# Performance work log

Measured on AMD Instinct MI355X. Metric: run time of the kernel, lower is better.

Reference implementation:

```python
import jax, jax.numpy as jnp
import numpy as np
import math

B, T, C, H = 2, 2048, 1024, 16
HD = C // H  # head_dim = 64


def setup_inputs() -> dict:
    key = jax.random.key(0)
    ks = jax.random.split(key, 10)
    s = 1.0 / math.sqrt(C)
    x = jax.random.normal(ks[0], (B, T, C), jnp.float32)
    wq = jax.random.normal(ks[1], (C, C), jnp.float32) * s
    wk = jax.random.normal(ks[2], (C, C), jnp.float32) * s
    wv = jax.random.normal(ks[3], (C, C), jnp.float32) * s
    wo = jax.random.normal(ks[4], (C, C), jnp.float32) * s
    bq = jnp.zeros((C,), jnp.float32)
    bk = jnp.zeros((C,), jnp.float32)
    bv = jnp.zeros((C,), jnp.float32)
    bo = jnp.zeros((C,), jnp.float32)
    fractal_dim = jnp.ones((1,), jnp.float32)  # scalar fractal dimension input
    alpha = jnp.asarray(1.5, jnp.float32)
    fractal_alpha_scale = jnp.asarray(0.5, jnp.float32)
    energy_normalizer = jnp.asarray(1.0, jnp.float32)
    return {"x": x, "fractal_dim": fractal_dim, "wq": wq, "bq": bq, "wk": wk,
            "bk": bk, "wv": wv, "bv": bv, "wo": wo, "bo": bo, "alpha": alpha,
            "fractal_alpha_scale": fractal_alpha_scale,
            "energy_normalizer": energy_normalizer}


def reference(x, fractal_dim, wq, bq, wk, bk, wv, bv, wo, bo, alpha,
              fractal_alpha_scale, energy_normalizer):
    b, t, c = x.shape
    # input energy: L2 norm over channels, [b, t, 1]
    input_energy = jnp.linalg.norm(x, axis=-1, keepdims=True)
    adaptive_alpha = alpha + fractal_alpha_scale * (fractal_dim - 1.5)  # [1]

    q = (x @ wq + bq).reshape(b, t, H, HD)
    k = (x @ wk + bk).reshape(b, t, H, HD)
    v = (x @ wv + bv).reshape(b, t, H, HD)

    # per-head FFT along the time axis -> complex64
    q_fft = jnp.fft.fft(q, axis=1)
    k_fft = jnp.fft.fft(k, axis=1)
    v_fft = jnp.fft.fft(v, axis=1)

    freqs = jnp.fft.fftfreq(t).astype(jnp.float32)  # [t]
    phase = adaptive_alpha * jnp.arctan(jnp.log(jnp.abs(freqs) + 1e-10))  # [t]
    # unit-modulus complex spectral filter, broadcast [1, t, 1, 1]
    filt = jax.lax.complex(jnp.cos(phase), jnp.sin(phase))[None, :, None, None]

    qf = q_fft * filt
    kf = k_fft * filt
    vf = v_fft * filt

    # real part of complex matmul Q_f @ K_f^T, computed without complex GEMM:
    # Re(qf kf^T) = qr kr^T - qi ki^T
    inv_sqrt = np.float32(1.0 / math.sqrt(HD))
    logits = (jnp.einsum('bthd,bshd->bhts', qf.real, kf.real)
              - jnp.einsum('bthd,bshd->bhts', qf.imag, kf.imag)) * inv_sqrt
    attn = jax.nn.softmax(logits, axis=-1)  # [b, h, t, s]

    # attn is real, so Re(attn @ vf) = attn @ Re(vf); out_proj has real weights
    # so taking the real part before the projection is exact.
    attended = jnp.einsum('bhts,bshd->bthd', attn, vf.real)
    out = attended.reshape(b, t, c) @ wo + bo

    out_energy = jnp.linalg.norm(out, axis=-1, keepdims=True)
    energy_ratio = input_energy / (out_energy + 1e-8)
    return out * energy_ratio * energy_normalizer
```

## Files before the change

### kernel.cpp

```cpp
#include <hip/hip_runtime.h>
#include <math.h>


typedef _Float16 half8 __attribute__((ext_vector_type(8)));
typedef float f32x4 __attribute__((ext_vector_type(4)));
#define MFMA16 __builtin_amdgcn_mfma_f32_16x16x32_f16

#define GLOAD16(g, l) __builtin_amdgcn_global_load_lds( \
    (const __attribute__((address_space(1))) void*)(g), \
    (__attribute__((address_space(3))) void*)(l), 16, 0, 0)

__device__ inline unsigned pack_split(float v) {
    _Float16 h = (_Float16)v;
    float r = (v - (float)h) * 2048.0f;
    _Float16 l = (_Float16)r;
    union { _Float16 f; unsigned short u; } a, b;
    a.f = h; b.f = l;
    return (unsigned)a.u | ((unsigned)b.u << 16);
}
__device__ inline void split2(float v, _Float16& h, _Float16& l) {
    h = (_Float16)v;
    l = (_Float16)((v - (float)h) * 2048.0f);
}
__device__ inline _Float16 lo16(unsigned u) {
    union { unsigned short s; _Float16 f; } x; x.s = (unsigned short)(u & 0xffffu); return x.f;
}
__device__ inline _Float16 hi16(unsigned u) {
    union { unsigned short s; _Float16 f; } x; x.s = (unsigned short)(u >> 16); return x.f;
}

__device__ inline void write_split(_Float16* dh, _Float16* dl, uint4 u0, uint4 u1) {
    uint4 lo, hi;
    lo.x = __builtin_amdgcn_perm(u0.y, u0.x, 0x05040100u);
    lo.y = __builtin_amdgcn_perm(u0.w, u0.z, 0x05040100u);
    lo.z = __builtin_amdgcn_perm(u1.y, u1.x, 0x05040100u);
    lo.w = __builtin_amdgcn_perm(u1.w, u1.z, 0x05040100u);
    hi.x = __builtin_amdgcn_perm(u0.y, u0.x, 0x07060302u);
    hi.y = __builtin_amdgcn_perm(u0.w, u0.z, 0x07060302u);
    hi.z = __builtin_amdgcn_perm(u1.y, u1.x, 0x07060302u);
    hi.w = __builtin_amdgcn_perm(u1.w, u1.z, 0x07060302u);
    *(uint4*)dh = lo;
    *(uint4*)dl = hi;
}

__global__ __launch_bounds__(256) void k_init_tables(
    float2* __restrict__ tw, float2* __restrict__ filt,
    const float* __restrict__ fd, const float* __restrict__ alpha,
    const float* __restrict__ fas)
{
    int i = blockIdx.x * 256 + threadIdx.x;
    double aa = (double)alpha[0] + (double)fas[0] * ((double)fd[0] - 1.5);
    if (i < 1024) {
        double ang = -2.0 * 3.14159265358979323846 * (double)i / 2048.0;
        double s, c;
        sincos(ang, &s, &c);
        tw[i] = make_float2((float)c, (float)s);
    }
    if (i < 2048) {
        double fr = (i < 1024) ? (double)i / 2048.0 : ((double)i - 2048.0) / 2048.0;
        double ph = aa * atan(log(fabs(fr) + 1e-10));
        double s, c;
        sincos(ph, &s, &c);
        filt[i] = make_float2((float)c, (float)s);
    }
}

__global__ __launch_bounds__(256) void k_prep_wpl3(
    const float* __restrict__ wq, const float* __restrict__ wk,
    const float* __restrict__ wv, _Float16* __restrict__ wpl)
{
    __shared__ float tile[64][65];
    const int z = blockIdx.z;
    const float* W = (z == 0) ? wq : (z == 1) ? wk : wv;
    _Float16* Whi = wpl + (size_t)z * 2097152;
    _Float16* Wlo = Whi + 1048576;
    const int kb = blockIdx.x * 64, cb = blockIdx.y * 64;
    const int t = threadIdx.x, r = t >> 4, c4 = (t & 15) * 4;
#pragma unroll
    for (int i = 0; i < 4; ++i) {
        int row = r + 16 * i;
        float4 v = *(const float4*)&W[(size_t)(kb + row) * 1024 + cb + c4];
        tile[row][c4 + 0] = v.x; tile[row][c4 + 1] = v.y;
        tile[row][c4 + 2] = v.z; tile[row][c4 + 3] = v.w;
    }
    __syncthreads();
#pragma unroll
    for (int h = 0; h < 2; ++h) {
        int idx = t + h * 256;
        int lane = idx & 63, kt2 = (idx >> 6) & 1, ct = idx >> 7;
        int cl = ct * 16 + (lane & 15);
        int kl = kt2 * 32 + ((lane >> 4) * 8);
        half8 hv, lv;
#pragma unroll
        for (int j = 0; j < 8; ++j) {
            _Float16 hh, ll;
            split2(tile[kl + j][cl], hh, ll);
            hv[j] = hh; lv[j] = ll;
        }
        size_t u = ((size_t)((cb >> 4) + ct) * 32 + (kb >> 5) + kt2) * 64 + lane;
        *(half8*)&Whi[u * 8] = hv;
        *(half8*)&Wlo[u * 8] = lv;
    }
}

__global__ __launch_bounds__(256) void k_prep_xpl(
    const float* __restrict__ x, _Float16* __restrict__ xpl)
{
    __shared__ float tile[64][65];
    _Float16* Xhi = xpl;
    _Float16* Xlo = xpl + 4194304;
    const int nb = blockIdx.x * 64, cb = blockIdx.y * 64;
    const int t = threadIdx.x, r = t >> 4, c4 = (t & 15) * 4;
#pragma unroll
    for (int i = 0; i < 4; ++i) {
        int row = r + 16 * i;
        float4 v = *(const float4*)&x[(size_t)(nb + row) * 1024 + cb + c4];
        tile[row][c4 + 0] = v.x; tile[row][c4 + 1] = v.y;
        tile[row][c4 + 2] = v.z; tile[row][c4 + 3] = v.w;
    }
    __syncthreads();
#pragma unroll
    for (int h = 0; h < 2; ++h) {
        int idx = t + h * 256;
        int lane = idx & 63, ct2 = (idx >> 6) & 1, ntl = (idx >> 7) & 3;
        int nl = ntl * 16 + (lane & 15);
        int cl = ct2 * 32 + ((lane >> 4) * 8);
        half8 hv, lv;
#pragma unroll
        for (int j = 0; j < 8; ++j) {
            _Float16 hh, ll;
            split2(tile[nl][cl + j], hh, ll);
            hv[j] = hh; lv[j] = ll;
        }
        size_t u = ((size_t)((nb >> 4) + ntl) * 32 + (cb >> 5) + ct2) * 64 + lane;
        *(half8*)&Xhi[u * 8] = hv;
        *(half8*)&Xlo[u * 8] = lv;
    }
}

__global__ __launch_bounds__(256) void k_prep_w(
    const float* __restrict__ W, unsigned* __restrict__ Wpk)
{
    __shared__ float tile[64][65];
    const int kb = blockIdx.x * 64, cb = blockIdx.y * 64;
    const int t = threadIdx.x, r = t >> 4, c4 = (t & 15) * 4;
#pragma unroll
    for (int i = 0; i < 4; ++i) {
        int row = r + 16 * i;
        float4 v = *(const float4*)&W[(size_t)(kb + row) * 1024 + cb + c4];
        tile[row][c4 + 0] = v.x; tile[row][c4 + 1] = v.y;
        tile[row][c4 + 2] = v.z; tile[row][c4 + 3] = v.w;
    }
    __syncthreads();
#pragma unroll
    for (int i = 0; i < 4; ++i) {
        int crow = r + 16 * i;
        uint4 o;
        o.x = pack_split(tile[c4 + 0][crow]);
        o.y = pack_split(tile[c4 + 1][crow]);
        o.z = pack_split(tile[c4 + 2][crow]);
        o.w = pack_split(tile[c4 + 3][crow]);
        *(uint4*)&Wpk[(size_t)(cb + crow) * 1024 + kb + c4] = o;
    }
}

__global__ __launch_bounds__(256) void k_gemm_qkv(
    const _Float16* __restrict__ xpl, const _Float16* __restrict__ wpl,
    const float* __restrict__ bq, const float* __restrict__ bk,
    const float* __restrict__ bv,
    float* __restrict__ qT, float* __restrict__ kT, float* __restrict__ vT)
{
    __shared__ __align__(16) _Float16 Ab[2][8][2][64][8];
    __shared__ __align__(16) _Float16 Bb[2][8][2][64][8];
    const int tid = threadIdx.x;
    const int mat = blockIdx.z;
    const _Float16* Ahi = wpl + (size_t)mat * 2097152;
    const _Float16* Alo = Ahi + 1048576;
    const _Float16* Bhi = xpl;
    const _Float16* Blo = xpl + 4194304;
    const float* bias = (mat == 0) ? bq : (mat == 1) ? bk : bv;
    float* outp       = (mat == 0) ? qT : (mat == 1) ? kT : vT;
    const int m0 = blockIdx.x * 128, n0 = blockIdx.y * 128;
    const int w = tid >> 6, lane = tid & 63, quad = lane >> 4, l15 = lane & 15;
    const int wm = (w & 1) * 4, wn = (w >> 1) * 4;

    const int s0 = 2 * w, s1 = 2 * w + 1;
    const size_t aT0 = (size_t)((m0 >> 4) + s0) * 32;
    const size_t aT1 = aT0 + 32;
    const size_t bT0 = (size_t)((n0 >> 4) + s0) * 32;
    const size_t bT1 = bT0 + 32;
    const int ln8 = lane * 8;

    f32x4 acc1[4][4], acc2[4][4];
    const f32x4 z4 = {0.f, 0.f, 0.f, 0.f};
#pragma unroll
    for (int i = 0; i < 4; ++i)
#pragma unroll
        for (int j = 0; j < 4; ++j) { acc1[i][j] = z4; acc2[i][j] = z4; }

    {
        size_t oA0 = aT0 * 512 + ln8;
        size_t oA1 = aT1 * 512 + ln8;
        size_t oB0 = bT0 * 512 + ln8;
        size_t oB1 = bT1 * 512 + ln8;
        GLOAD16(Ahi + oA0, &Ab[0][s0][0][0][0]);
        GLOAD16(Alo + oA0, &Ab[0][s0][1][0][0]);
        GLOAD16(Ahi + oA1, &Ab[0][s1][0][0][0]);
        GLOAD16(Alo + oA1, &Ab[0][s1][1][0][0]);
        GLOAD16(Bhi + oB0, &Bb[0][s0][0][0][0]);
        GLOAD16(Blo + oB0, &Bb[0][s0][1][0][0]);
        GLOAD16(Bhi + oB1, &Bb[0][s1][0][0][0]);
        GLOAD16(Blo + oB1, &Bb[0][s1][1][0][0]);
    }
    __syncthreads();

    for (int kt = 0; kt < 32; ++kt) {
        const int cur = kt & 1, nxt = cur ^ 1;
        if (kt < 31) {
            int kn = kt + 1;
            size_t oA0 = (aT0 + kn) * 512 + ln8;
            size_t oA1 = (aT1 + kn) * 512 + ln8;
            size_t oB0 = (bT0 + kn) * 512 + ln8;
            size_t oB1 = (bT1 + kn) * 512 + ln8;
            GLOAD16(Ahi + oA0, &Ab[nxt][s0][0][0][0]);
            GLOAD16(Alo + oA0, &Ab[nxt][s0][1][0][0]);
            GLOAD16(Ahi + oA1, &Ab[nxt][s1][0][0][0]);
            GLOAD16(Alo + oA1, &Ab[nxt][s1][1][0][0]);
            GLOAD16(Bhi + oB0, &Bb[nxt][s0][0][0][0]);
            GLOAD16(Blo + oB0, &Bb[nxt][s0][1][0][0]);
            GLOAD16(Bhi + oB1, &Bb[nxt][s1][0][0][0]);
            GLOAD16(Blo + oB1, &Bb[nxt][s1][1][0][0]);
        }
        half8 ah[4], al[4];
#pragma unroll
        for (int mt = 0; mt < 4; ++mt) {
            ah[mt] = *(half8*)&Ab[cur][wm + mt][0][lane][0];
            al[mt] = *(half8*)&Ab[cur][wm + mt][1][lane][0];
        }
#pragma unroll
        for (int nt = 0; nt < 4; ++nt) {
            half8 bh = *(half8*)&Bb[cur][wn + nt][0][lane][0];
            half8 bl = *(half8*)&Bb[cur][wn + nt][1][lane][0];
#pragma unroll
            for (int mt = 0; mt < 4; ++mt) {
                acc1[mt][nt] = MFMA16(ah[mt], bh, acc1[mt][nt], 0, 0, 0);
                acc2[mt][nt] = MFMA16(ah[mt], bl, acc2[mt][nt], 0, 0, 0);
                acc2[mt][nt] = MFMA16(al[mt], bh, acc2[mt][nt], 0, 0, 0);
            }
        }
        __syncthreads();
    }
    const int b_ = n0 >> 11, t0 = n0 & 2047;
#pragma unroll
    for (int mt = 0; mt < 4; ++mt) {
#pragma unroll
        for (int r_ = 0; r_ < 4; ++r_) {
            int m = m0 + (wm + mt) * 16 + quad * 4 + r_;
            float bs = bias[m];
            float* orow = &outp[(size_t)(b_ * 1024 + m) * 2048 + t0];
#pragma unroll
            for (int nt = 0; nt < 4; ++nt) {
                float val = acc1[mt][nt][r_] + acc2[mt][nt][r_] * (1.f / 2048.f) + bs;
                orow[(wn + nt) * 16 + l15] = val;
            }
        }
    }
}

__global__ __launch_bounds__(256) void k_fft_filter(
    float* __restrict__ qT, float* __restrict__ kT, float* __restrict__ vT,
    float* __restrict__ qiT, float* __restrict__ kiT,
    const float2* __restrict__ tw, const float2* __restrict__ filt)
{
    __shared__ float2 sf[2048];
    const int bid = blockIdx.x;
    const int mat = bid >> 10;
    const int pair = bid & 1023;
    const int seq0 = pair * 2, seq1 = seq0 + 1;
    float* base = (mat == 0) ? qT : (mat == 1) ? kT : vT;
    float* src0 = base + (size_t)seq0 * 2048;
    float* src1 = base + (size_t)seq1 * 2048;
    const int tid = threadIdx.x;

    for (int i = tid; i < 2048; i += 256) {
        int j = (int)(__brev((unsigned)i) >> 21);
        sf[j] = make_float2(src0[i], src1[i]);
    }
    __syncthreads();
    for (int st = 1; st <= 11; ++st) {
        const int half = 1 << (st - 1);
        const int shift = 11 - st;
        for (int u = tid; u < 1024; u += 256) {
            int pos = u & (half - 1);
            int bi = 2 * u - pos;
            float2 w = tw[pos << shift];
            float2 a = sf[bi], b = sf[bi + half];
            float tr = w.x * b.x - w.y * b.y;
            float ti = w.x * b.y + w.y * b.x;
            sf[bi]        = make_float2(a.x + tr, a.y + ti);
            sf[bi + half] = make_float2(a.x - tr, a.y - ti);
        }
        __syncthreads();
    }
    unsigned* dr0 = (unsigned*)src0;
    unsigned* dr1 = (unsigned*)src1;
    unsigned* di0 = (mat == 0) ? (unsigned*)(qiT + (size_t)seq0 * 2048)
                               : (unsigned*)(kiT + (size_t)seq0 * 2048);
    unsigned* di1 = (mat == 0) ? (unsigned*)(qiT + (size_t)seq1 * 2048)
                               : (unsigned*)(kiT + (size_t)seq1 * 2048);
    for (int i = tid; i < 2048; i += 256) {
        float2 z  = sf[i];
        float2 zm = sf[(2048 - i) & 2047];
        float Are = 0.5f * (z.x + zm.x), Aim = 0.5f * (z.y - zm.y);
        float Bre = 0.5f * (z.y + zm.y), Bim = 0.5f * (zm.x - z.x);
        float2 f = filt[i];
        float re0 = Are * f.x - Aim * f.y, im0 = Are * f.y + Aim * f.x;
        float re1 = Bre * f.x - Bim * f.y, im1 = Bre * f.y + Bim * f.x;
        if (mat == 0) {
            dr0[i] = pack_split(0.125f * re0); di0[i] = pack_split(0.125f * im0);
            dr1[i] = pack_split(0.125f * re1); di1[i] = pack_split(0.125f * im1);
        } else if (mat == 1) {
            dr0[i] = pack_split(re0); di0[i] = pack_split(-im0);
            dr1[i] = pack_split(re1); di1[i] = pack_split(-im1);
        } else {
            dr0[i] = pack_split(re0);
            dr1[i] = pack_split(re1);
        }
    }
}

__global__ __launch_bounds__(512, 2) void k_flash(
    const unsigned* __restrict__ qpk, const unsigned* __restrict__ qipk,
    const unsigned* __restrict__ kpk, const unsigned* __restrict__ kipk,
    const unsigned* __restrict__ vpk, unsigned* __restrict__ attpk)
{
    __shared__ __align__(16) _Float16 Kbuf[2][4][4][2][64][8];
    __shared__ __align__(16) _Float16 Vbuf[2][2][4][2][64][8];

    const int tid = threadIdx.x;
    const int w = tid >> 6, lane = tid & 63;
    const int quad = lane >> 4, l15 = lane & 15;
    const int p = blockIdx.x;
    const int bh = (p & 7) * 4 + (p >> 6);
    const int tb = (p >> 3) & 7;
    const size_t bc = (size_t)bh * 64;
    const int tw0 = tb * 256 + w * 16;

    half8 aqh[2][4], aql[2][4];
#pragma unroll
    for (int rg = 0; rg < 2; ++rg) {
#pragma unroll
        for (int kc = 0; kc < 4; ++kc) {
#pragma unroll
            for (int j = 0; j < 8; ++j) {
                int d = kc * 32 + quad * 8 + j;
                int t = tw0 + rg * 128 + l15;
                unsigned u = (d < 64) ? qpk[(bc + d) * 2048 + t]
                                      : qipk[(bc + d - 64) * 2048 + t];
                aqh[rg][kc][j] = lo16(u);
                aql[rg][kc][j] = hi16(u);
            }
        }
    }

    f32x4 O1[2][4], O2[2][4];
    const f32x4 zero4 = {0.f, 0.f, 0.f, 0.f};
#pragma unroll
    for (int rg = 0; rg < 2; ++rg)
#pragma unroll
        for (int nt = 0; nt < 4; ++nt) { O1[rg][nt] = zero4; O2[rg][nt] = zero4; }
    float m_[2] = {-3e38f, -3e38f};
    float l_[2] = {0.f, 0.f};

    const int sK = tid & 63;
    const int dc0 = tid >> 6;
    const int stK = sK >> 4;
    const int kcK0 = dc0 >> 2;
    const int laneK = (sK & 15) + ((dc0 & 3) << 4);
    const unsigned* kre = &kpk[(bc + dc0 * 8) * 2048 + sK];
    const unsigned* kim = &kipk[(bc + dc0 * 8) * 2048 + sK];
    const int sc2V = tid >> 8;
    const int ntV = (tid >> 6) & 3, laneV = tid & 63;
    const int dV = ntV * 16 + (laneV & 15);
    const int s0V = sc2V * 32 + (laneV >> 4) * 4;
    const unsigned* vbase = &vpk[(bc + dV) * 2048 + s0V];

    unsigned ka0, ka1, ka2, ka3, ka4, ka5, ka6, ka7;
    unsigned kb0, kb1, kb2, kb3, kb4, kb5, kb6, kb7;
    uint4 va0, va1;
    ka0 = kre[0 * 2048]; ka1 = kre[1 * 2048];
    ka2 = kre[2 * 2048]; ka3 = kre[3 * 2048];
    ka4 = kre[4 * 2048]; ka5 = kre[5 * 2048];
    ka6 = kre[6 * 2048]; ka7 = kre[7 * 2048];
    kb0 = kim[0 * 2048]; kb1 = kim[1 * 2048];
    kb2 = kim[2 * 2048]; kb3 = kim[3 * 2048];
    kb4 = kim[4 * 2048]; kb5 = kim[5 * 2048];
    kb6 = kim[6 * 2048]; kb7 = kim[7 * 2048];
    va0 = *(const uint4*)vbase;
    va1 = *(const uint4*)(vbase + 16);
    write_split(&Kbuf[0][stK][kcK0][0][laneK][0], &Kbuf[0][stK][kcK0][1][laneK][0],
                make_uint4(ka0, ka1, ka2, ka3), make_uint4(ka4, ka5, ka6, ka7));
    write_split(&Kbuf[0][stK][kcK0 + 2][0][laneK][0], &Kbuf[0][stK][kcK0 + 2][1][laneK][0],
                make_uint4(kb0, kb1, kb2, kb3), make_uint4(kb4, kb5, kb6, kb7));
    write_split(&Vbuf[0][sc2V][ntV][0][laneV][0], &Vbuf[0][sc2V][ntV][1][laneV][0],
                va0, va1);
    kre += 64; kim += 64; vbase += 64;
    ka0 = kre[0 * 2048]; ka1 = kre[1 * 2048];
    ka2 = kre[2 * 2048]; ka3 = kre[3 * 2048];
    ka4 = kre[4 * 2048]; ka5 = kre[5 * 2048];
    ka6 = kre[6 * 2048]; ka7 = kre[7 * 2048];
    kb0 = kim[0 * 2048]; kb1 = kim[1 * 2048];
    kb2 = kim[2 * 2048]; kb3 = kim[3 * 2048];
    kb4 = kim[4 * 2048]; kb5 = kim[5 * 2048];
    kb6 = kim[6 * 2048]; kb7 = kim[7 * 2048];
    va0 = *(const uint4*)vbase;
    va1 = *(const uint4*)(vbase + 16);
    __syncthreads();

    for (int it = 0; it < 32; ++it) {
        const int cur = it & 1, nxt = cur ^ 1;
        if (it < 31) {
            write_split(&Kbuf[nxt][stK][kcK0][0][laneK][0],
                        &Kbuf[nxt][stK][kcK0][1][laneK][0],
                        make_uint4(ka0, ka1, ka2, ka3), make_uint4(ka4, ka5, ka6, ka7));
            write_split(&Kbuf[nxt][stK][kcK0 + 2][0][laneK][0],
                        &Kbuf[nxt][stK][kcK0 + 2][1][laneK][0],
                        make_uint4(kb0, kb1, kb2, kb3), make_uint4(kb4, kb5, kb6, kb7));
            write_split(&Vbuf[nxt][sc2V][ntV][0][laneV][0],
                        &Vbuf[nxt][sc2V][ntV][1][laneV][0], va0, va1);
        }
        if (it < 30) {
            kre += 64; kim += 64; vbase += 64;
            ka0 = kre[0 * 2048]; ka1 = kre[1 * 2048];
            ka2 = kre[2 * 2048]; ka3 = kre[3 * 2048];
            ka4 = kre[4 * 2048]; ka5 = kre[5 * 2048];
            ka6 = kre[6 * 2048]; ka7 = kre[7 * 2048];
            kb0 = kim[0 * 2048]; kb1 = kim[1 * 2048];
            kb2 = kim[2 * 2048]; kb3 = kim[3 * 2048];
            kb4 = kim[4 * 2048]; kb5 = kim[5 * 2048];
            kb6 = kim[6 * 2048]; kb7 = kim[7 * 2048];
            va0 = *(const uint4*)vbase;
            va1 = *(const uint4*)(vbase + 16);
        }

        f32x4 S1[2][4], S2[2][4];
#pragma unroll
        for (int rg = 0; rg < 2; ++rg)
#pragma unroll
            for (int st = 0; st < 4; ++st) { S1[rg][st] = zero4; S2[rg][st] = zero4; }
        __builtin_amdgcn_s_setprio(1);
#pragma unroll
        for (int st = 0; st < 4; ++st) {
#pragma unroll
            for (int kc = 0; kc < 4; ++kc) {
                half8 khf = *(half8*)&Kbuf[cur][st][kc][0][lane][0];
                half8 klf = *(half8*)&Kbuf[cur][st][kc][1][lane][0];
#pragma unroll
                for (int rg = 0; rg < 2; ++rg) {
                    S1[rg][st] = MFMA16(khf, aqh[rg][kc], S1[rg][st], 0, 0, 0);
                    S2[rg][st] = MFMA16(klf, aqh[rg][kc], S2[rg][st], 0, 0, 0);
                    S2[rg][st] = MFMA16(khf, aql[rg][kc], S2[rg][st], 0, 0, 0);
                }
            }
        }
        __builtin_amdgcn_s_setprio(0);

        half8 pb[2][2];
#pragma unroll
        for (int rg = 0; rg < 2; ++rg) {
#pragma unroll
            for (int st = 0; st < 4; ++st)
                S1[rg][st] = S1[rg][st] + S2[rg][st] * (1.f / 2048.f);
            float mt = -3e38f;
#pragma unroll
            for (int st = 0; st < 4; ++st)
#pragma unroll
                for (int r = 0; r < 4; ++r)
                    mt = fmaxf(mt, S1[rg][st][r]);
            mt = fmaxf(mt, __shfl_xor(mt, 16));
            mt = fmaxf(mt, __shfl_xor(mt, 32));
            if (!__all(mt <= m_[rg] + 8.f)) {
                float mn2 = fmaxf(m_[rg], mt);
                float al = __expf(m_[rg] - mn2);
                m_[rg] = mn2;
                l_[rg] *= al;
#pragma unroll
                for (int nt = 0; nt < 4; ++nt) { O1[rg][nt] *= al; O2[rg][nt] *= al; }
            }
            float mn = m_[rg];
            float rs = 0.f;
            _Float16 ph[4][4];
#pragma unroll
            for (int st = 0; st < 4; ++st)
#pragma unroll
                for (int r = 0; r < 4; ++r) {
                    float pe = __expf(S1[rg][st][r] - mn);
                    rs += pe;
                    ph[st][r] = (_Float16)pe;
                }
            rs += __shfl_xor(rs, 16);
            rs += __shfl_xor(rs, 32);
            l_[rg] += rs;
#pragma unroll
            for (int sc2 = 0; sc2 < 2; ++sc2) {
                half8 t8;
                t8[0] = ph[2 * sc2][0];     t8[1] = ph[2 * sc2][1];
                t8[2] = ph[2 * sc2][2];     t8[3] = ph[2 * sc2][3];
                t8[4] = ph[2 * sc2 + 1][0]; t8[5] = ph[2 * sc2 + 1][1];
                t8[6] = ph[2 * sc2 + 1][2]; t8[7] = ph[2 * sc2 + 1][3];
                pb[rg][sc2] = t8;
            }
        }

        __builtin_amdgcn_s_setprio(1);
#pragma unroll
        for (int sc2 = 0; sc2 < 2; ++sc2) {
#pragma unroll
            for (int nt = 0; nt < 4; ++nt) {
                half8 vh = *(half8*)&Vbuf[cur][sc2][nt][0][lane][0];
                half8 vl = *(half8*)&Vbuf[cur][sc2][nt][1][lane][0];
                O1[0][nt] = MFMA16(vh, pb[0][sc2], O1[0][nt], 0, 0, 0);
                O2[0][nt] = MFMA16(vl, pb[0][sc2], O2[0][nt], 0, 0, 0);
                O1[1][nt] = MFMA16(vh, pb[1][sc2], O1[1][nt], 0, 0, 0);
                O2[1][nt] = MFMA16(vl, pb[1][sc2], O2[1][nt], 0, 0, 0);
            }
        }
        __builtin_amdgcn_s_setprio(0);

        __syncthreads();
    }

    const int b = bh >> 4, h = bh & 15;
#pragma unroll
    for (int rg = 0; rg < 2; ++rg) {
        float inv = 1.0f / l_[rg];
        int t = tw0 + rg * 128 + l15;
        size_t row = (size_t)b * 2048 + t;
#pragma unroll
        for (int nt = 0; nt < 4; ++nt) {
#pragma unroll
            for (int r = 0; r < 4; ++r) {
                float val = (O1[rg][nt][r] + O2[rg][nt][r] * (1.f / 2048.f)) * inv;
                attpk[row * 1024 + h * 64 + nt * 16 + quad * 4 + r] = pack_split(val);
            }
        }
    }
}

__global__ __launch_bounds__(256) void k_gemm_out(
    const unsigned* __restrict__ attpk, const unsigned* __restrict__ wopk,
    const float* __restrict__ bo, float* __restrict__ out)
{
    __shared__ __align__(16) _Float16 Ab[8][2][64][8];
    __shared__ __align__(16) _Float16 Bb[8][2][64][8];
    const int tid = threadIdx.x;
    const int m0 = blockIdx.x * 128, n0 = blockIdx.y * 128;
    const int w = tid >> 6, lane = tid & 63, quad = lane >> 4, l15 = lane & 15;
    const int wm = (w & 1) * 4, wn = (w >> 1) * 4;

    const int chA = tid & 3, rA = tid >> 2;
    const int flA = (rA & 15) + 16 * chA, mtA = rA >> 4;
    const unsigned* gA0 = &attpk[(size_t)(m0 + rA) * 1024 + chA * 8];
    const unsigned* gA1 = gA0 + (size_t)64 * 1024;
    const unsigned* gB0 = &wopk[(size_t)(n0 + rA) * 1024 + chA * 8];
    const unsigned* gB1 = gB0 + (size_t)64 * 1024;

    uint4 pa0 = *(const uint4*)gA0, pa1 = *(const uint4*)(gA0 + 4);
    uint4 pa2 = *(const uint4*)gA1, pa3 = *(const uint4*)(gA1 + 4);
    uint4 pb0 = *(const uint4*)gB0, pb1 = *(const uint4*)(gB0 + 4);
    uint4 pb2 = *(const uint4*)gB1, pb3 = *(const uint4*)(gB1 + 4);

    f32x4 acc1[4][4], acc2[4][4];
    const f32x4 z4 = {0.f, 0.f, 0.f, 0.f};
#pragma unroll
    for (int i = 0; i < 4; ++i)
#pragma unroll
        for (int j = 0; j < 4; ++j) { acc1[i][j] = z4; acc2[i][j] = z4; }

    for (int k0 = 0; k0 < 1024; k0 += 32) {
        __syncthreads();
        write_split(&Ab[mtA][0][flA][0],     &Ab[mtA][1][flA][0],     pa0, pa1);
        write_split(&Ab[mtA + 4][0][flA][0], &Ab[mtA + 4][1][flA][0], pa2, pa3);
        write_split(&Bb[mtA][0][flA][0],     &Bb[mtA][1][flA][0],     pb0, pb1);
        write_split(&Bb[mtA + 4][0][flA][0], &Bb[mtA + 4][1][flA][0], pb2, pb3);
        __syncthreads();
        if (k0 < 992) {
            int kn = k0 + 32;
            pa0 = *(const uint4*)(gA0 + kn); pa1 = *(const uint4*)(gA0 + kn + 4);
            pa2 = *(const uint4*)(gA1 + kn); pa3 = *(const uint4*)(gA1 + kn + 4);
            pb0 = *(const uint4*)(gB0 + kn); pb1 = *(const uint4*)(gB0 + kn + 4);
            pb2 = *(const uint4*)(gB1 + kn); pb3 = *(const uint4*)(gB1 + kn + 4);
        }
        half8 ah[4], al[4];
#pragma unroll
        for (int mt = 0; mt < 4; ++mt) {
            ah[mt] = *(half8*)&Ab[wm + mt][0][lane][0];
            al[mt] = *(half8*)&Ab[wm + mt][1][lane][0];
        }
#pragma unroll
        for (int nt = 0; nt < 4; ++nt) {
            half8 bh = *(half8*)&Bb[wn + nt][0][lane][0];
            half8 bl = *(half8*)&Bb[wn + nt][1][lane][0];
#pragma unroll
            for (int mt = 0; mt < 4; ++mt) {
                acc1[mt][nt] = MFMA16(ah[mt], bh, acc1[mt][nt], 0, 0, 0);
                acc2[mt][nt] = MFMA16(ah[mt], bl, acc2[mt][nt], 0, 0, 0);
                acc2[mt][nt] = MFMA16(al[mt], bh, acc2[mt][nt], 0, 0, 0);
            }
        }
    }
#pragma unroll
    for (int mt = 0; mt < 4; ++mt) {
#pragma unroll
        for (int r_ = 0; r_ < 4; ++r_) {
            int m = m0 + (wm + mt) * 16 + quad * 4 + r_;
            float* orow = &out[(size_t)m * 1024 + n0];
#pragma unroll
            for (int nt = 0; nt < 4; ++nt) {
                int n = (wn + nt) * 16 + l15;
                float val = acc1[mt][nt][r_] + acc2[mt][nt][r_] * (1.f / 2048.f)
                          + bo[n0 + n];
                orow[n] = val;
            }
        }
    }
}

__global__ __launch_bounds__(256) void k_norm(
    const float* __restrict__ x, float* __restrict__ out,
    const float* __restrict__ en)
{
    const int row = blockIdx.x;
    const int tid = threadIdx.x;
    const float* xr = x + (size_t)row * 1024;
    float* orow = out + (size_t)row * 1024;
    float4 xv = *(const float4*)&xr[tid * 4];
    float4 ov = *(const float4*)&orow[tid * 4];
    float ssx = xv.x * xv.x + xv.y * xv.y + xv.z * xv.z + xv.w * xv.w;
    float sso = ov.x * ov.x + ov.y * ov.y + ov.z * ov.z + ov.w * ov.w;
#pragma unroll
    for (int m = 1; m <= 32; m <<= 1) {
        ssx += __shfl_xor(ssx, m, 64);
        sso += __shfl_xor(sso, m, 64);
    }
    __shared__ float rx[4], ro[4];
    const int wid = tid >> 6;
    if ((tid & 63) == 0) { rx[wid] = ssx; ro[wid] = sso; }
    __syncthreads();
    float tsx = rx[0] + rx[1] + rx[2] + rx[3];
    float tso = ro[0] + ro[1] + ro[2] + ro[3];
    float scale = sqrtf(tsx) / (sqrtf(tso) + 1e-8f) * en[0];
    ov.x *= scale; ov.y *= scale; ov.z *= scale; ov.w *= scale;
    *(float4*)&orow[tid * 4] = ov;
}

extern "C" void kernel_launch(void* const* d_in, const int* in_sizes, int n_in,
                              void* d_out, int out_size, void* d_ws, size_t ws_size,
                              hipStream_t stream)
{
    const float* x     = (const float*)d_in[0];
    const float* fd    = (const float*)d_in[1];
    const float* wq    = (const float*)d_in[2];
    const float* bq    = (const float*)d_in[3];
    const float* wk    = (const float*)d_in[4];
    const float* bk    = (const float*)d_in[5];
    const float* wv    = (const float*)d_in[6];
    const float* bv    = (const float*)d_in[7];
    const float* wo    = (const float*)d_in[8];
    const float* bo    = (const float*)d_in[9];
    const float* alpha = (const float*)d_in[10];
    const float* fas   = (const float*)d_in[11];
    const float* en    = (const float*)d_in[12];
    float* out = (float*)d_out;
    float* ws  = (float*)d_ws;

    float* qT  = ws;
    float* kT  = ws + (size_t)1 * 4194304;
    float* vT  = ws + (size_t)2 * 4194304;
    float* qiT = ws + (size_t)3 * 4194304;
    float* kiT = ws + (size_t)4 * 4194304;
    float* att = ws + (size_t)5 * 4194304;
    float2* tw   = (float2*)(ws + (size_t)6 * 4194304);
    float2* filt = (float2*)(ws + (size_t)6 * 4194304 + 2048);

    _Float16* wpl = (_Float16*)qiT;
    _Float16* xpl = (_Float16*)att;
    unsigned* attpk  = (unsigned*)att;
    unsigned* wopk   = (unsigned*)qT;

    k_init_tables<<<8, 256, 0, stream>>>(tw, filt, fd, alpha, fas);
    k_prep_wpl3<<<dim3(16, 16, 3), 256, 0, stream>>>(wq, wk, wv, wpl);
    k_prep_xpl<<<dim3(64, 16), 256, 0, stream>>>(x, xpl);
    k_gemm_qkv<<<dim3(8, 32, 3), 256, 0, stream>>>(xpl, wpl, bq, bk, bv,
                                                   qT, kT, vT);
    k_fft_filter<<<3072, 256, 0, stream>>>(qT, kT, vT, qiT, kiT, tw, filt);
    k_flash<<<256, 512, 0, stream>>>((const unsigned*)qT, (const unsigned*)qiT,
                                     (const unsigned*)kT, (const unsigned*)kiT,
                                     (const unsigned*)vT, attpk);
    k_prep_w<<<dim3(16, 16), 256, 0, stream>>>(wo, wopk);
    k_gemm_out<<<dim3(32, 8), 256, 0, stream>>>(attpk, wopk, bo, out);
    k_norm<<<4096, 256, 0, stream>>>(x, out, en);
}
```

Measured before the change: 424.5 us.

## Use MFMA-tiled planar fp16 layout for out-proj GEMM and radix-4 FFT stages

```diff
diff --git a/kernel.cpp b/kernel.cpp
--- a/kernel.cpp
+++ b/kernel.cpp
@@ -3,6 +3,7 @@
 
 
 typedef _Float16 half8 __attribute__((ext_vector_type(8)));
+typedef _Float16 half4 __attribute__((ext_vector_type(4)));
 typedef float f32x4 __attribute__((ext_vector_type(4)));
 #define MFMA16 __builtin_amdgcn_mfma_f32_16x16x32_f16
 
@@ -10,23 +11,25 @@
     (const __attribute__((address_space(1))) void*)(g), \
     (__attribute__((address_space(3))) void*)(l), 16, 0, 0)
 
+__device__ inline void split2(float v, _Float16& h, _Float16& l) {
+    h = (_Float16)v;
+    l = (_Float16)((v - (float)h) * 2048.0f);
+}
 __device__ inline unsigned pack_split(float v) {
-    _Float16 h = (_Float16)v;
-    float r = (v - (float)h) * 2048.0f;
-    _Float16 l = (_Float16)r;
+    _Float16 h, l;
+    split2(v, h, l);
     union { _Float16 f; unsigned short u; } a, b;
     a.f = h; b.f = l;
     return (unsigned)a.u | ((unsigned)b.u << 16);
 }
-__device__ inline void split2(float v, _Float16& h, _Float16& l) {
-    h = (_Float16)v;
-    l = (_Float16)((v - (float)h) * 2048.0f);
-}
 __device__ inline _Float16 lo16(unsigned u) {
     union { unsigned short s; _Float16 f; } x; x.s = (unsigned short)(u & 0xffffu); return x.f;
 }
 __device__ inline _Float16 hi16(unsigned u) {
     union { unsigned short s; _Float16 f; } x; x.s = (unsigned short)(u >> 16); return x.f;
+}
+__device__ inline float2 cmul(float2 a, float2 b) {
+    return make_float2(a.x * b.x - a.y * b.y, a.x * b.y + a.y * b.x);
 }
 
 __device__ inline void write_split(_Float16* dh, _Float16* dl, uint4 u0, uint4 u1) {
@@ -103,6 +106,41 @@
     }
 }
 
+__global__ __launch_bounds__(256) void k_prep_wpl1(
+    const float* __restrict__ W, _Float16* __restrict__ wpl)
+{
+    __shared__ float tile[64][65];
+    _Float16* Whi = wpl;
+    _Float16* Wlo = wpl + 1048576;
+    const int kb = blockIdx.x * 64, cb = blockIdx.y * 64;
+    const int t = threadIdx.x, r = t >> 4, c4 = (t & 15) * 4;
+#pragma unroll
+    for (int i = 0; i < 4; ++i) {
+        int row = r + 16 * i;
+        float4 v = *(const float4*)&W[(size_t)(kb + row) * 1024 + cb + c4];
+        tile[row][c4 + 0] = v.x; tile[row][c4 + 1] = v.y;
+        tile[row][c4 + 2] = v.z; tile[row][c4 + 3] = v.w;
+    }
+    __syncthreads();
+#pragma unroll
+    for (int h = 0; h < 2; ++h) {
+        int idx = t + h * 256;
+        int lane = idx & 63, kt2 = (idx >> 6) & 1, ct = idx >> 7;
+        int cl = ct * 16 + (lane & 15);
+        int kl = kt2 * 32 + ((lane >> 4) * 8);
+        half8 hv, lv;
+#pragma unroll
+        for (int j = 0; j < 8; ++j) {
+            _Float16 hh, ll;
+            split2(tile[kl + j][cl], hh, ll);
+            hv[j] = hh; lv[j] = ll;
+        }
+        size_t u = ((size_t)((cb >> 4) + ct) * 32 + (kb >> 5) + kt2) * 64 + lane;
+        *(half8*)&Whi[u * 8] = hv;
+        *(half8*)&Wlo[u * 8] = lv;
+    }
+}
+
 __global__ __launch_bounds__(256) void k_prep_xpl(
     const float* __restrict__ x, _Float16* __restrict__ xpl)
 {
@@ -135,32 +173,6 @@
         size_t u = ((size_t)((nb >> 4) + ntl) * 32 + (cb >> 5) + ct2) * 64 + lane;
         *(half8*)&Xhi[u * 8] = hv;
         *(half8*)&Xlo[u * 8] = lv;
-    }
-}
-
-__global__ __launch_bounds__(256) void k_prep_w(
-    const float* __restrict__ W, unsigned* __restrict__ Wpk)
-{
-    __shared__ float tile[64][65];
-    const int kb = blockIdx.x * 64, cb = blockIdx.y * 64;
-    const int t = threadIdx.x, r = t >> 4, c4 = (t & 15) * 4;
-#pragma unroll
-    for (int i = 0; i < 4; ++i) {
-        int row = r + 16 * i;
-        float4 v = *(const float4*)&W[(size_t)(kb + row) * 1024 + cb + c4];
-        tile[row][c4 + 0] = v.x; tile[row][c4 + 1] = v.y;
-        tile[row][c4 + 2] = v.z; tile[row][c4 + 3] = v.w;
-    }
-    __syncthreads();
-#pragma unroll
-    for (int i = 0; i < 4; ++i) {
-        int crow = r + 16 * i;
-        uint4 o;
-        o.x = pack_split(tile[c4 + 0][crow]);
-        o.y = pack_split(tile[c4 + 1][crow]);
-        o.z = pack_split(tile[c4 + 2][crow]);
-        o.w = pack_split(tile[c4 + 3][crow]);
-        *(uint4*)&Wpk[(size_t)(cb + crow) * 1024 + kb + c4] = o;
     }
 }
 
@@ -287,21 +299,41 @@
         sf[j] = make_float2(src0[i], src1[i]);
     }
     __syncthreads();
-    for (int st = 1; st <= 11; ++st) {
-        const int half = 1 << (st - 1);
-        const int shift = 11 - st;
-        for (int u = tid; u < 1024; u += 256) {
-            int pos = u & (half - 1);
-            int bi = 2 * u - pos;
-            float2 w = tw[pos << shift];
-            float2 a = sf[bi], b = sf[bi + half];
-            float tr = w.x * b.x - w.y * b.y;
-            float ti = w.x * b.y + w.y * b.x;
-            sf[bi]        = make_float2(a.x + tr, a.y + ti);
-            sf[bi + half] = make_float2(a.x - tr, a.y - ti);
+#pragma unroll
+    for (int st = 1; st <= 9; st += 2) {
+        const int h = 1 << (st - 1);
+        const int s = 11 - st;
+        for (int u = tid; u < 512; u += 256) {
+            int m = u & (h - 1);
+            int g = u >> (st - 1);
+            int bi = g * 4 * h + m;
+            float2 a = sf[bi], b = sf[bi + h], c = sf[bi + 2 * h], d = sf[bi + 3 * h];
+            float2 W  = tw[m << s];
+            float2 W2 = tw[m << (s - 1)];
+            float2 wb = cmul(W, b), wd = cmul(W, d);
+            float2 a1 = make_float2(a.x + wb.x, a.y + wb.y);
+            float2 b1 = make_float2(a.x - wb.x, a.y - wb.y);
+            float2 c1 = make_float2(c.x + wd.x, c.y + wd.y);
+            float2 d1 = make_float2(c.x - wd.x, c.y - wd.y);
+            float2 w2c = cmul(W2, c1);
+            float2 w2d = cmul(W2, d1);
+            float2 w3d = make_float2(w2d.y, -w2d.x);
+            sf[bi]         = make_float2(a1.x + w2c.x, a1.y + w2c.y);
+            sf[bi + 2 * h] = make_float2(a1.x - w2c.x, a1.y - w2c.y);
+            sf[bi + h]     = make_float2(b1.x + w3d.x, b1.y + w3d.y);
+            sf[bi + 3 * h] = make_float2(b1.x - w3d.x, b1.y - w3d.y);
         }
         __syncthreads();
     }
+    for (int u = tid; u < 1024; u += 256) {
+        float2 w = tw[u];
+        float2 a = sf[u], b = sf[u + 1024];
+        float2 wb = cmul(w, b);
+        sf[u]        = make_float2(a.x + wb.x, a.y + wb.y);
+        sf[u + 1024] = make_float2(a.x - wb.x, a.y - wb.y);
+    }
+    __syncthreads();
+
     unsigned* dr0 = (unsigned*)src0;
     unsigned* dr1 = (unsigned*)src1;
     unsigned* di0 = (mat == 0) ? (unsigned*)(qiT + (size_t)seq0 * 2048)
@@ -332,7 +364,7 @@
 __global__ __launch_bounds__(512, 2) void k_flash(
     const unsigned* __restrict__ qpk, const unsigned* __restrict__ qipk,
     const unsigned* __restrict__ kpk, const unsigned* __restrict__ kipk,
-    const unsigned* __restrict__ vpk, unsigned* __restrict__ attpk)
+    const unsigned* __restrict__ vpk, _Float16* __restrict__ attpl)
 {
     __shared__ __align__(16) _Float16 Kbuf[2][4][4][2][64][8];
     __shared__ __align__(16) _Float16 Vbuf[2][2][4][2][64][8];
@@ -534,41 +566,48 @@
 #pragma unroll
     for (int rg = 0; rg < 2; ++rg) {
         float inv = 1.0f / l_[rg];
-        int t = tw0 + rg * 128 + l15;
-        size_t row = (size_t)b * 2048 + t;
+        int mrow = b * 2048 + tw0 + rg * 128 + l15;
+        size_t mt32 = (size_t)(mrow >> 4) * 32;
 #pragma unroll
         for (int nt = 0; nt < 4; ++nt) {
+            size_t u = (mt32 + h * 2 + (nt >> 1)) * 512
+                     + (size_t)(l15 + 16 * ((nt * 2 + (quad >> 1)) & 3)) * 8
+                     + (quad & 1) * 4;
+            half4 hv, lv;
 #pragma unroll
             for (int r = 0; r < 4; ++r) {
                 float val = (O1[rg][nt][r] + O2[rg][nt][r] * (1.f / 2048.f)) * inv;
-                attpk[row * 1024 + h * 64 + nt * 16 + quad * 4 + r] = pack_split(val);
-            }
+                _Float16 hh, ll;
+                split2(val, hh, ll);
+                hv[r] = hh; lv[r] = ll;
+            }
+            *(half4*)&attpl[u] = hv;
+            *(half4*)&attpl[4194304 + u] = lv;
         }
     }
 }
 
 __global__ __launch_bounds__(256) void k_gemm_out(
-    const unsigned* __restrict__ attpk, const unsigned* __restrict__ wopk,
+    const _Float16* __restrict__ attpl, const _Float16* __restrict__ wopl,
     const float* __restrict__ bo, float* __restrict__ out)
 {
-    __shared__ __align__(16) _Float16 Ab[8][2][64][8];
-    __shared__ __align__(16) _Float16 Bb[8][2][64][8];
+    __shared__ __align__(16) _Float16 Ab[2][8][2][64][8];
+    __shared__ __align__(16) _Float16 Bb[2][8][2][64][8];
     const int tid = threadIdx.x;
+    const _Float16* Ahi = attpl;
+    const _Float16* Alo = attpl + 4194304;
+    const _Float16* Bhi = wopl;
+    const _Float16* Blo = wopl + 1048576;
     const int m0 = blockIdx.x * 128, n0 = blockIdx.y * 128;
     const int w = tid >> 6, lane = tid & 63, quad = lane >> 4, l15 = lane & 15;
     const int wm = (w & 1) * 4, wn = (w >> 1) * 4;
 
-    const int chA = tid & 3, rA = tid >> 2;
-    const int flA = (rA & 15) + 16 * chA, mtA = rA >> 4;
-    const unsigned* gA0 = &attpk[(size_t)(m0 + rA) * 1024 + chA * 8];
-    const unsigned* gA1 = gA0 + (size_t)64 * 1024;
-    const unsigned* gB0 = &wopk[(size_t)(n0 + rA) * 1024 + chA * 8];
-    const unsigned* gB1 = gB0 + (size_t)64 * 1024;
-
-    uint4 pa0 = *(const uint4*)gA0, pa1 = *(const uint4*)(gA0 + 4);
-    uint4 pa2 = *(const uint4*)gA1, pa3 = *(const uint4*)(gA1 + 4);
-    uint4 pb0 = *(const uint4*)gB0, pb1 = *(const uint4*)(gB0 + 4);
-    uint4 pb2 = *(const uint4*)gB1, pb3 = *(const uint4*)(gB1 + 4);
+    const int s0 = 2 * w, s1 = 2 * w + 1;
+    const size_t aT0 = (size_t)((m0 >> 4) + s0) * 32;
+    const size_t aT1 = aT0 + 32;
+    const size_t bT0 = (size_t)((n0 >> 4) + s0) * 32;
+    const size_t bT1 = bT0 + 32;
+    const int ln8 = lane * 8;
 
     f32x4 acc1[4][4], acc2[4][4];
     const f32x4 z4 = {0.f, 0.f, 0.f, 0.f};
@@ -577,30 +616,49 @@
 #pragma unroll
         for (int j = 0; j < 4; ++j) { acc1[i][j] = z4; acc2[i][j] = z4; }
 
-    for (int k0 = 0; k0 < 1024; k0 += 32) {
-        __syncthreads();
-        write_split(&Ab[mtA][0][flA][0],     &Ab[mtA][1][flA][0],     pa0, pa1);
-        write_split(&Ab[mtA + 4][0][flA][0], &Ab[mtA + 4][1][flA][0], pa2, pa3);
-        write_split(&Bb[mtA][0][flA][0],     &Bb[mtA][1][flA][0],     pb0, pb1);
-        write_split(&Bb[mtA + 4][0][flA][0], &Bb[mtA + 4][1][flA][0], pb2, pb3);
-        __syncthreads();
-        if (k0 < 992) {
-            int kn = k0 + 32;
-            pa0 = *(const uint4*)(gA0 + kn); pa1 = *(const uint4*)(gA0 + kn + 4);
-            pa2 = *(const uint4*)(gA1 + kn); pa3 = *(const uint4*)(gA1 + kn + 4);
-            pb0 = *(const uint4*)(gB0 + kn); pb1 = *(const uint4*)(gB0 + kn + 4);
-            pb2 = *(const uint4*)(gB1 + kn); pb3 = *(const uint4*)(gB1 + kn + 4);
+    {
+        size_t oA0 = aT0 * 512 + ln8;
+        size_t oA1 = aT1 * 512 + ln8;
+        size_t oB0 = bT0 * 512 + ln8;
+        size_t oB1 = bT1 * 512 + ln8;
+        GLOAD16(Ahi + oA0, &Ab[0][s0][0][0][0]);
+        GLOAD16(Alo + oA0, &Ab[0][s0][1][0][0]);
+        GLOAD16(Ahi + oA1, &Ab[0][s1][0][0][0]);
+        GLOAD16(Alo + oA1, &Ab[0][s1][1][0][0]);
+        GLOAD16(Bhi + oB0, &Bb[0][s0][0][0][0]);
+        GLOAD16(Blo + oB0, &Bb[0][s0][1][0][0]);
+        GLOAD16(Bhi + oB1, &Bb[0][s1][0][0][0]);
+        GLOAD16(Blo + oB1, &Bb[0][s1][1][0][0]);
+    }
+    __syncthreads();
+
+    for (int kt = 0; kt < 32; ++kt) {
+        const int cur = kt & 1, nxt = cur ^ 1;
+        if (kt < 31) {
+            int kn = kt + 1;
+            size_t oA0 = (aT0 + kn) * 512 + ln8;
+            size_t oA1 = (aT1 + kn) * 512 + ln8;
+            size_t oB0 = (bT0 + kn) * 512 + ln8;
+            size_t oB1 = (bT1 + kn) * 512 + ln8;
+            GLOAD16(Ahi + oA0, &Ab[nxt][s0][0][0][0]);
+            GLOAD16(Alo + oA0, &Ab[nxt][s0][1][0][0]);
+            GLOAD16(Ahi + oA1, &Ab[nxt][s1][0][0][0]);
+            GLOAD16(Alo + oA1, &Ab[nxt][s1][1][0][0]);
+            GLOAD16(Bhi + oB0, &Bb[nxt][s0][0][0][0]);
+            GLOAD16(Blo + oB0, &Bb[nxt][s0][1][0][0]);
+            GLOAD16(Bhi + oB1, &Bb[nxt][s1][0][0][0]);
+            GLOAD16(Blo + oB1, &Bb[nxt][s1][1][0][0]);
         }
         half8 ah[4], al[4];
 #pragma unroll
         for (int mt = 0; mt < 4; ++mt) {
-            ah[mt] = *(half8*)&Ab[wm + mt][0][lane][0];
-            al[mt] = *(half8*)&Ab[wm + mt][1][lane][0];
+            ah[mt] = *(half8*)&Ab[cur][wm + mt][0][lane][0];
+            al[mt] = *(half8*)&Ab[cur][wm + mt][1][lane][0];
         }
 #pragma unroll
         for (int nt = 0; nt < 4; ++nt) {
-            half8 bh = *(half8*)&Bb[wn + nt][0][lane][0];
-            half8 bl = *(half8*)&Bb[wn + nt][1][lane][0];
+            half8 bh = *(half8*)&Bb[cur][wn + nt][0][lane][0];
+            half8 bl = *(half8*)&Bb[cur][wn + nt][1][lane][0];
 #pragma unroll
             for (int mt = 0; mt < 4; ++mt) {
                 acc1[mt][nt] = MFMA16(ah[mt], bh, acc1[mt][nt], 0, 0, 0);
@@ -608,6 +666,7 @@
                 acc2[mt][nt] = MFMA16(al[mt], bh, acc2[mt][nt], 0, 0, 0);
             }
         }
+        __syncthreads();
     }
 #pragma unroll
     for (int mt = 0; mt < 4; ++mt) {
@@ -683,10 +742,10 @@
     float2* tw   = (float2*)(ws + (size_t)6 * 4194304);
     float2* filt = (float2*)(ws + (size_t)6 * 4194304 + 2048);
 
-    _Float16* wpl = (_Float16*)qiT;
-    _Float16* xpl = (_Float16*)att;
-    unsigned* attpk  = (unsigned*)att;
-    unsigned* wopk   = (unsigned*)qT;
+    _Float16* wpl   = (_Float16*)qiT;
+    _Float16* xpl   = (_Float16*)att;
+    _Float16* attpl = (_Float16*)att;
+    _Float16* wopl  = (_Float16*)qT;
 
     k_init_tables<<<8, 256, 0, stream>>>(tw, filt, fd, alpha, fas);
     k_prep_wpl3<<<dim3(16, 16, 3), 256, 0, stream>>>(wq, wk, wv, wpl);
@@ -696,8 +755,8 @@
     k_fft_filter<<<3072, 256, 0, stream>>>(qT, kT, vT, qiT, kiT, tw, filt);
     k_flash<<<256, 512, 0, stream>>>((const unsigned*)qT, (const unsigned*)qiT,
                                      (const unsigned*)kT, (const unsigned*)kiT,
-                                     (const unsigned*)vT, attpk);
-    k_prep_w<<<dim3(16, 16), 256, 0, stream>>>(wo, wopk);
-    k_gemm_out<<<dim3(32, 8), 256, 0, stream>>>(attpk, wopk, bo, out);
+                                     (const unsigned*)vT, attpl);
+    k_prep_wpl1<<<dim3(16, 16), 256, 0, stream>>>(wo, wopl);
+    k_gemm_out<<<dim3(32, 8), 256, 0, stream>>>(attpl, wopl, bo, out);
     k_norm<<<4096, 256, 0, stream>>>(x, out, en);
 }
```

Result: no change. 423.4 us (-0.3%).
